# Optimization experiments

Hardware: AMD Instinct MI355X
Metric: run time of the kernel (lower is better)

## Reference

```python
import jax, jax.numpy as jnp
import numpy as np

B, V_IN, V_OUT, C_IN, C_OUT, SPIRAL, K_NNZ = 4, 12500, 50000, 64, 32, 9, 3

def setup_inputs() -> dict:
    key = jax.random.key(0)
    k1, k2, k3, k4, k5 = jax.random.split(key, 5)
    x = jax.random.normal(k1, (B, V_IN, C_IN), dtype=jnp.float32)
    spiral_indices = jax.random.randint(k2, (V_OUT, SPIRAL), 0, V_OUT)
    up_idx = jax.random.randint(k3, (V_OUT, K_NNZ), 0, V_IN)
    up_val = jax.random.uniform(k4, (V_OUT, K_NNZ), dtype=jnp.float32)
    weight = jax.random.normal(k5, (SPIRAL * C_IN, C_OUT), dtype=jnp.float32) / np.sqrt(SPIRAL * C_IN)
    bias = jnp.zeros((C_OUT,), dtype=jnp.float32)
    return {"x": x, "spiral_indices": spiral_indices, "up_idx": up_idx,
            "up_val": up_val, "weight": weight, "bias": bias}

def reference(x, spiral_indices, up_idx, up_val, weight, bias):
    # pool_bvc: sparse up_transform @ x, 3 nnz per output vertex
    # x: [B, V_in, C]; up_idx/up_val: [V_out, K]
    up = jnp.einsum('bvkc,vk->bvc', x[:, up_idx], up_val)  # [B, V_out, C_in]
    # SpiralConv: gather spiral neighborhoods, flatten, linear
    g = up[:, spiral_indices]                               # [B, V_out, S, C_in]
    g = g.reshape(g.shape[0], g.shape[1], -1)               # [B, V_out, S*C_in]
    y = jnp.einsum('bvf,fo->bvo', g, weight) + bias         # [B, V_out, C_out]
    return jax.nn.relu(y)
```

## Files before the change

### kernel.cpp

```cpp
#include <hip/hip_runtime.h>
#include <hip/hip_bf16.h>

#define B_     4
#define V_IN   12500
#define V_OUT  50000
#define C_IN   64
#define C_OUT  32
#define SPIRAL 9
#define K_NNZ  3
#define ROWS   (B_ * V_OUT)
#define KDIM   (SPIRAL * C_IN)
#define KSTEPS (KDIM / 32)
#define WFRAG_ELEMS (KSTEPS * 2 * 64 * 8)

#define GROUPS_PER_B (V_OUT / 16)
#define G1           2048
#define TILES_PER_B  782
#define G2           1024

typedef __attribute__((ext_vector_type(8))) short short8_t;
typedef __attribute__((ext_vector_type(4))) float floatx4;

__device__ __forceinline__ unsigned short f32_to_bf16(float f) {
    unsigned int u = __float_as_uint(f);
    unsigned int r = u + 0x7fffu + ((u >> 16) & 1u);
    return (unsigned short)(r >> 16);
}

__global__ __launch_bounds__(256) void upsample_kernel(
    const float* __restrict__ x,
    const int* __restrict__ up_idx,
    const float* __restrict__ up_val,
    const float* __restrict__ weight,
    unsigned short* __restrict__ up_bf16,
    unsigned short* __restrict__ w_frag)
{
    int tid = threadIdx.x;
    if (blockIdx.x == G1) {
        for (int idx = tid; idx < WFRAG_ELEMS; idx += 256) {
            int j     = idx & 7;
            int lane  = (idx >> 3) & 63;
            int ntile = (idx >> 9) & 1;
            int kstep = idx >> 10;
            int k = kstep * 32 + (lane >> 4) * 8 + j;
            int n = ntile * 16 + (lane & 15);
            w_frag[idx] = f32_to_bf16(weight[k * C_OUT + n]);
        }
        return;
    }
    int xcd = blockIdx.x & 7;
    int b   = xcd >> 1;
    int h   = xcd & 1;
    int j   = blockIdx.x >> 3;
    int lane16 = tid & 15;
    int sub    = tid >> 4;

    const float* xb = x + (size_t)b * V_IN * C_IN;
    unsigned short* upb = up_bf16 + (size_t)b * V_OUT * C_IN;

    for (int gl = h + 2 * j; gl < GROUPS_PER_B; gl += 512) {
        int v = gl * 16 + sub;
        const int*   ui = up_idx + v * K_NNZ;
        const float* uv = up_val + v * K_NNZ;
        float a0 = 0.f, a1 = 0.f, a2 = 0.f, a3 = 0.f;
#pragma unroll
        for (int k = 0; k < K_NNZ; k++) {
            int u = ui[k];
            float val = uv[k];
            const float4* xp = (const float4*)(xb + (size_t)u * C_IN) + lane16;
            float4 xv = *xp;
            a0 += val * xv.x; a1 += val * xv.y; a2 += val * xv.z; a3 += val * xv.w;
        }
        ushort4 o;
        o.x = f32_to_bf16(a0); o.y = f32_to_bf16(a1);
        o.z = f32_to_bf16(a2); o.w = f32_to_bf16(a3);
        *((ushort4*)(upb + (size_t)v * C_IN) + lane16) = o;
    }
}

__global__ __launch_bounds__(256) void gemm_kernel(
    const unsigned short* __restrict__ up_bf16,
    const int* __restrict__ spiral,
    const unsigned short* __restrict__ w_frag,
    const float* __restrict__ bias,
    float* __restrict__ out)
{
    __shared__ __align__(16) unsigned short w_lds[WFRAG_ELEMS];
    int tid = threadIdx.x;
    {
        const uint4* src = (const uint4*)w_frag;
        uint4* dst = (uint4*)w_lds;
#pragma unroll
        for (int i = 0; i < WFRAG_ELEMS / 8 / 256; i++)
            dst[tid + i * 256] = src[tid + i * 256];
    }
    __syncthreads();

    int wave = tid >> 6;
    int lane = tid & 63;
    int m    = lane & 15;
    int quad = lane >> 4;

    int xcd = blockIdx.x & 7;
    int b   = xcd >> 1;
    int h   = xcd & 1;
    int j   = blockIdx.x >> 3;

    const unsigned short* upb = up_bf16 + (size_t)b * V_OUT * C_IN;
    float* outb = out + (size_t)b * V_OUT * C_OUT;

    float4 bias0 = ((const float4*)bias)[quad];
    float4 bias1 = ((const float4*)bias)[4 + quad];

    for (int tl = h + 2 * j; tl < TILES_PER_B; tl += 256) {
        int vr = tl * 64 + wave * 16 + m;
        int valid = vr < V_OUT;
        int v = valid ? vr : 0;
        const int* sp = spiral + v * SPIRAL;

        short8_t g0[SPIRAL], g1[SPIRAL];
#pragma unroll
        for (int s = 0; s < SPIRAL; s++) {
            const unsigned short* rowp = upb + (size_t)sp[s] * C_IN;
            g0[s] = *(const short8_t*)(rowp + quad * 8);
            g1[s] = *(const short8_t*)(rowp + 32 + quad * 8);
        }

        floatx4 acc0 = {0.f, 0.f, 0.f, 0.f};
        floatx4 acc1 = {0.f, 0.f, 0.f, 0.f};
#pragma unroll
        for (int kstep = 0; kstep < KSTEPS; kstep++) {
            short8_t gf = (kstep & 1) ? g1[kstep >> 1] : g0[kstep >> 1];
            const short8_t* wp0 = (const short8_t*)(w_lds + ((kstep * 2 + 0) * 64 + lane) * 8);
            const short8_t* wp1 = (const short8_t*)(w_lds + ((kstep * 2 + 1) * 64 + lane) * 8);
            acc0 = __builtin_amdgcn_mfma_f32_16x16x32_bf16(*wp0, gf, acc0, 0, 0, 0);
            acc1 = __builtin_amdgcn_mfma_f32_16x16x32_bf16(*wp1, gf, acc1, 0, 0, 0);
        }

        if (valid) {
            float4 o0, o1;
            o0.x = acc0[0] + bias0.x; o0.y = acc0[1] + bias0.y;
            o0.z = acc0[2] + bias0.z; o0.w = acc0[3] + bias0.w;
            o1.x = acc1[0] + bias1.x; o1.y = acc1[1] + bias1.y;
            o1.z = acc1[2] + bias1.z; o1.w = acc1[3] + bias1.w;
            o0.x = o0.x > 0.f ? o0.x : 0.f;  o0.y = o0.y > 0.f ? o0.y : 0.f;
            o0.z = o0.z > 0.f ? o0.z : 0.f;  o0.w = o0.w > 0.f ? o0.w : 0.f;
            o1.x = o1.x > 0.f ? o1.x : 0.f;  o1.y = o1.y > 0.f ? o1.y : 0.f;
            o1.z = o1.z > 0.f ? o1.z : 0.f;  o1.w = o1.w > 0.f ? o1.w : 0.f;
            float* op = outb + (size_t)vr * C_OUT;
            *(float4*)(op + quad * 4)      = o0;
            *(float4*)(op + 16 + quad * 4) = o1;
        }
    }
}

extern "C" void kernel_launch(void* const* d_in, const int* in_sizes, int n_in,
                              void* d_out, int out_size, void* d_ws, size_t ws_size,
                              hipStream_t stream) {
    const float* x      = (const float*)d_in[0];
    const int*   spiral = (const int*)d_in[1];
    const int*   up_idx = (const int*)d_in[2];
    const float* up_val = (const float*)d_in[3];
    const float* weight = (const float*)d_in[4];
    const float* bias   = (const float*)d_in[5];
    float* out = (float*)d_out;

    unsigned short* up_ws  = (unsigned short*)d_ws;
    unsigned short* w_frag = up_ws + (size_t)ROWS * C_IN;

    upsample_kernel<<<G1 + 1, 256, 0, stream>>>(x, up_idx, up_val, weight, up_ws, w_frag);
    gemm_kernel<<<G2, 256, 0, stream>>>(up_ws, spiral, w_frag, bias, out);
}
```

Baseline: 130.9 us.

## Software-pipeline gathers in upsample and spiral GEMM kernels with double buffering

The upsample kernel now prefetches the next group's sparse indices and values while the current group's x rows are gathered. The GEMM kernel halves its grid and double-buffers spiral indices and gathered bf16 rows, so the next tile's loads are in flight while MFMAs run on the current tile. The aim is to hide dependent gather latency. In exchange it raises register pressure, with launch bounds set to 2 blocks per CU, and gives fewer blocks for the scheduler to balance.

Result: slower. 173.3 us (+32.4%).

```diff
diff --git a/kernel.cpp b/kernel.cpp
--- a/kernel.cpp
+++ b/kernel.cpp
@@ -16,7 +16,7 @@
 #define GROUPS_PER_B (V_OUT / 16)
 #define G1           2048
 #define TILES_PER_B  782
-#define G2           1024
+#define G2           512
 
 typedef __attribute__((ext_vector_type(8))) short short8_t;
 typedef __attribute__((ext_vector_type(4))) float floatx4;
@@ -52,33 +52,95 @@
     int b   = xcd >> 1;
     int h   = xcd & 1;
     int j   = blockIdx.x >> 3;
+    int slot = h + 2 * j;
     int lane16 = tid & 15;
     int sub    = tid >> 4;
 
     const float* xb = x + (size_t)b * V_IN * C_IN;
     unsigned short* upb = up_bf16 + (size_t)b * V_OUT * C_IN;
 
-    for (int gl = h + 2 * j; gl < GROUPS_PER_B; gl += 512) {
-        int v = gl * 16 + sub;
-        const int*   ui = up_idx + v * K_NNZ;
-        const float* uv = up_val + v * K_NNZ;
-        float a0 = 0.f, a1 = 0.f, a2 = 0.f, a3 = 0.f;
-#pragma unroll
-        for (int k = 0; k < K_NNZ; k++) {
-            int u = ui[k];
-            float val = uv[k];
-            const float4* xp = (const float4*)(xb + (size_t)u * C_IN) + lane16;
-            float4 xv = *xp;
-            a0 += val * xv.x; a1 += val * xv.y; a2 += val * xv.z; a3 += val * xv.w;
+    int gl = slot;
+    if (gl >= GROUPS_PER_B) return;
+    int v = gl * 16 + sub;
+    int   u0 = up_idx[v * K_NNZ + 0], u1 = up_idx[v * K_NNZ + 1], u2 = up_idx[v * K_NNZ + 2];
+    float c0 = up_val[v * K_NNZ + 0], c1 = up_val[v * K_NNZ + 1], c2 = up_val[v * K_NNZ + 2];
+
+    while (true) {
+        int gln = gl + 512;
+        int un0 = 0, un1 = 0, un2 = 0; float cn0 = 0, cn1 = 0, cn2 = 0;
+        if (gln < GROUPS_PER_B) {
+            int vn = gln * 16 + sub;
+            un0 = up_idx[vn * K_NNZ + 0]; un1 = up_idx[vn * K_NNZ + 1]; un2 = up_idx[vn * K_NNZ + 2];
+            cn0 = up_val[vn * K_NNZ + 0]; cn1 = up_val[vn * K_NNZ + 1]; cn2 = up_val[vn * K_NNZ + 2];
         }
+        float4 x0 = *((const float4*)(xb + (size_t)u0 * C_IN) + lane16);
+        float4 x1 = *((const float4*)(xb + (size_t)u1 * C_IN) + lane16);
+        float4 x2 = *((const float4*)(xb + (size_t)u2 * C_IN) + lane16);
+        float a0 = c0 * x0.x + c1 * x1.x + c2 * x2.x;
+        float a1 = c0 * x0.y + c1 * x1.y + c2 * x2.y;
+        float a2 = c0 * x0.z + c1 * x1.z + c2 * x2.z;
+        float a3 = c0 * x0.w + c1 * x1.w + c2 * x2.w;
         ushort4 o;
         o.x = f32_to_bf16(a0); o.y = f32_to_bf16(a1);
         o.z = f32_to_bf16(a2); o.w = f32_to_bf16(a3);
-        *((ushort4*)(upb + (size_t)v * C_IN) + lane16) = o;
-    }
-}
-
-__global__ __launch_bounds__(256) void gemm_kernel(
+        *((ushort4*)(upb + (size_t)(gl * 16 + sub) * C_IN) + lane16) = o;
+        if (gln >= GROUPS_PER_B) break;
+        gl = gln;
+        u0 = un0; u1 = un1; u2 = un2; c0 = cn0; c1 = cn1; c2 = cn2;
+    }
+}
+
+__device__ __forceinline__ void load_sp(int* dst, const int* __restrict__ spiral,
+                                        int t, int wave, int m) {
+    int vr = t * 64 + wave * 16 + m;
+    int v = vr < V_OUT ? vr : 0;
+    const int* sp = spiral + v * SPIRAL;
+#pragma unroll
+    for (int s = 0; s < SPIRAL; s++) dst[s] = sp[s];
+}
+
+__device__ __forceinline__ void load_g(short8_t (*g)[2], const int* sp,
+                                       const unsigned short* __restrict__ upb, int quad) {
+#pragma unroll
+    for (int s = 0; s < SPIRAL; s++) {
+        const unsigned short* rowp = upb + (size_t)sp[s] * C_IN;
+        g[s][0] = *(const short8_t*)(rowp + quad * 8);
+        g[s][1] = *(const short8_t*)(rowp + 32 + quad * 8);
+    }
+}
+
+__device__ __forceinline__ void compute_store(const short8_t (*g)[2],
+    const unsigned short* w_lds, int t, int wave, int lane, int m, int quad,
+    float4 bias0, float4 bias1, float* __restrict__ outb)
+{
+    floatx4 acc0 = {0.f, 0.f, 0.f, 0.f};
+    floatx4 acc1 = {0.f, 0.f, 0.f, 0.f};
+#pragma unroll
+    for (int kstep = 0; kstep < KSTEPS; kstep++) {
+        short8_t gf = g[kstep >> 1][kstep & 1];
+        const short8_t* wp0 = (const short8_t*)(w_lds + ((kstep * 2 + 0) * 64 + lane) * 8);
+        const short8_t* wp1 = (const short8_t*)(w_lds + ((kstep * 2 + 1) * 64 + lane) * 8);
+        acc0 = __builtin_amdgcn_mfma_f32_16x16x32_bf16(*wp0, gf, acc0, 0, 0, 0);
+        acc1 = __builtin_amdgcn_mfma_f32_16x16x32_bf16(*wp1, gf, acc1, 0, 0, 0);
+    }
+    int vr = t * 64 + wave * 16 + m;
+    if (vr < V_OUT) {
+        float4 o0, o1;
+        o0.x = acc0[0] + bias0.x; o0.y = acc0[1] + bias0.y;
+        o0.z = acc0[2] + bias0.z; o0.w = acc0[3] + bias0.w;
+        o1.x = acc1[0] + bias1.x; o1.y = acc1[1] + bias1.y;
+        o1.z = acc1[2] + bias1.z; o1.w = acc1[3] + bias1.w;
+        o0.x = o0.x > 0.f ? o0.x : 0.f;  o0.y = o0.y > 0.f ? o0.y : 0.f;
+        o0.z = o0.z > 0.f ? o0.z : 0.f;  o0.w = o0.w > 0.f ? o0.w : 0.f;
+        o1.x = o1.x > 0.f ? o1.x : 0.f;  o1.y = o1.y > 0.f ? o1.y : 0.f;
+        o1.z = o1.z > 0.f ? o1.z : 0.f;  o1.w = o1.w > 0.f ? o1.w : 0.f;
+        float* op = outb + (size_t)vr * C_OUT;
+        *(float4*)(op + quad * 4)      = o0;
+        *(float4*)(op + 16 + quad * 4) = o1;
+    }
+}
+
+__global__ __launch_bounds__(256, 2) void gemm_kernel(
     const unsigned short* __restrict__ up_bf16,
     const int* __restrict__ spiral,
     const unsigned short* __restrict__ w_frag,
@@ -101,10 +163,11 @@
     int m    = lane & 15;
     int quad = lane >> 4;
 
-    int xcd = blockIdx.x & 7;
-    int b   = xcd >> 1;
-    int h   = xcd & 1;
-    int j   = blockIdx.x >> 3;
+    int xcd  = blockIdx.x & 7;
+    int b    = xcd >> 1;
+    int h    = xcd & 1;
+    int j    = blockIdx.x >> 3;
+    int slot = h + 2 * j;
 
     const unsigned short* upb = up_bf16 + (size_t)b * V_OUT * C_IN;
     float* outb = out + (size_t)b * V_OUT * C_OUT;
@@ -112,45 +175,24 @@
     float4 bias0 = ((const float4*)bias)[quad];
     float4 bias1 = ((const float4*)bias)[4 + quad];
 
-    for (int tl = h + 2 * j; tl < TILES_PER_B; tl += 256) {
-        int vr = tl * 64 + wave * 16 + m;
-        int valid = vr < V_OUT;
-        int v = valid ? vr : 0;
-        const int* sp = spiral + v * SPIRAL;
-
-        short8_t g0[SPIRAL], g1[SPIRAL];
-#pragma unroll
-        for (int s = 0; s < SPIRAL; s++) {
-            const unsigned short* rowp = upb + (size_t)sp[s] * C_IN;
-            g0[s] = *(const short8_t*)(rowp + quad * 8);
-            g1[s] = *(const short8_t*)(rowp + 32 + quad * 8);
-        }
-
-        floatx4 acc0 = {0.f, 0.f, 0.f, 0.f};
-        floatx4 acc1 = {0.f, 0.f, 0.f, 0.f};
-#pragma unroll
-        for (int kstep = 0; kstep < KSTEPS; kstep++) {
-            short8_t gf = (kstep & 1) ? g1[kstep >> 1] : g0[kstep >> 1];
-            const short8_t* wp0 = (const short8_t*)(w_lds + ((kstep * 2 + 0) * 64 + lane) * 8);
-            const short8_t* wp1 = (const short8_t*)(w_lds + ((kstep * 2 + 1) * 64 + lane) * 8);
-            acc0 = __builtin_amdgcn_mfma_f32_16x16x32_bf16(*wp0, gf, acc0, 0, 0, 0);
-            acc1 = __builtin_amdgcn_mfma_f32_16x16x32_bf16(*wp1, gf, acc1, 0, 0, 0);
-        }
-
-        if (valid) {
-            float4 o0, o1;
-            o0.x = acc0[0] + bias0.x; o0.y = acc0[1] + bias0.y;
-            o0.z = acc0[2] + bias0.z; o0.w = acc0[3] + bias0.w;
-            o1.x = acc1[0] + bias1.x; o1.y = acc1[1] + bias1.y;
-            o1.z = acc1[2] + bias1.z; o1.w = acc1[3] + bias1.w;
-            o0.x = o0.x > 0.f ? o0.x : 0.f;  o0.y = o0.y > 0.f ? o0.y : 0.f;
-            o0.z = o0.z > 0.f ? o0.z : 0.f;  o0.w = o0.w > 0.f ? o0.w : 0.f;
-            o1.x = o1.x > 0.f ? o1.x : 0.f;  o1.y = o1.y > 0.f ? o1.y : 0.f;
-            o1.z = o1.z > 0.f ? o1.z : 0.f;  o1.w = o1.w > 0.f ? o1.w : 0.f;
-            float* op = outb + (size_t)vr * C_OUT;
-            *(float4*)(op + quad * 4)      = o0;
-            *(float4*)(op + 16 + quad * 4) = o1;
-        }
+    int nt = (TILES_PER_B - 1 - slot) / 128 + 1;
+
+    int      spb[2][SPIRAL];
+    short8_t gb[2][SPIRAL][2];
+    load_sp(spb[0], spiral, slot, wave, m);
+    load_sp(spb[1], spiral, slot + 128, wave, m);
+    load_g(gb[0], spb[0], upb, quad);
+
+    int i = 0;
+    while (true) {
+        if (i + 1 < nt) load_g(gb[1], spb[1], upb, quad);
+        if (i + 2 < nt) load_sp(spb[0], spiral, slot + (i + 2) * 128, wave, m);
+        compute_store(gb[0], w_lds, slot + i * 128, wave, lane, m, quad, bias0, bias1, outb);
+        if (++i == nt) break;
+        if (i + 1 < nt) load_g(gb[0], spb[0], upb, quad);
+        if (i + 2 < nt) load_sp(spb[1], spiral, slot + (i + 2) * 128, wave, m);
+        compute_store(gb[1], w_lds, slot + i * 128, wave, lane, m, quad, bias0, bias1, outb);
+        if (++i == nt) break;
     }
 }
 
```
